# Optimization experiments

Hardware: AMD Instinct MI355X
Metric: run time of the kernel (lower is better)

## Reference

```python
import jax, jax.numpy as jnp
import numpy as np

N = 32768
NIN = 12
NC = 16
HID = 512
K = 8
B = 3.0
L = 8
D_HALF = NIN // 2                      # 6
DIN = D_HALF + NC                      # conditioner input
DOUT = (3 * K - 1) * (NIN - D_HALF)    # conditioner output
MIN_W = 1e-3
MIN_H = 1e-3
MIN_D = 1e-3
DERIV_CONST = float(np.log(np.exp(1.0 - MIN_D) - 1.0))  # softplus^{-1}(1-min_d)


def setup_inputs() -> dict:
    key = jax.random.key(0)
    ks = jax.random.split(key, 12)
    z = jax.random.normal(ks[0], (N, NIN), dtype=jnp.float32)
    c = jax.random.normal(ks[1], (N, NC), dtype=jnp.float32)

    def lin(k, fan_in, shape):
        bound = 1.0 / np.sqrt(fan_in)
        return jax.random.uniform(k, shape, jnp.float32, -bound, bound)

    W0 = lin(ks[2], DIN, (L, DIN, HID)); b0 = lin(ks[3], DIN, (L, HID))
    W1 = lin(ks[4], HID, (L, HID, HID)); b1 = lin(ks[5], HID, (L, HID))
    W2 = lin(ks[6], HID, (L, HID, HID)); b2 = lin(ks[7], HID, (L, HID))
    W3 = lin(ks[8], HID, (L, HID, DOUT)); b3 = lin(ks[9], HID, (L, DOUT))

    rng = np.random.default_rng(0)
    perms = jnp.asarray(np.stack([rng.permutation(NIN) for _ in range(L - 1)]),
                        dtype=jnp.int32)  # [L-1, NIN]
    return dict(z=z, c=c, W0=W0, b0=b0, W1=W1, b1=b1, W2=W2, b2=b2,
                W3=W3, b3=b3, perms=perms)


def _rqs(x, uw, uh, ud):
    """Unconstrained rational-quadratic spline (forward).
    x: [N, d2]; uw/uh: [N, d2, K]; ud: [N, d2, K+1] (already edge-padded)."""
    widths = jax.nn.softmax(uw, axis=-1)
    widths = MIN_W + (1.0 - MIN_W * K) * widths
    cw = jnp.cumsum(widths, axis=-1)
    cw = jnp.concatenate([jnp.zeros_like(cw[..., :1]), cw], axis=-1)
    cw = 2.0 * B * cw - B
    cw = cw.at[..., 0].set(-B).at[..., -1].set(B)
    w = cw[..., 1:] - cw[..., :-1]

    heights = jax.nn.softmax(uh, axis=-1)
    heights = MIN_H + (1.0 - MIN_H * K) * heights
    ch = jnp.cumsum(heights, axis=-1)
    ch = jnp.concatenate([jnp.zeros_like(ch[..., :1]), ch], axis=-1)
    ch = 2.0 * B * ch - B
    ch = ch.at[..., 0].set(-B).at[..., -1].set(B)
    h = ch[..., 1:] - ch[..., :-1]

    d = MIN_D + jax.nn.softplus(ud)  # [N, d2, K+1]

    xc = jnp.clip(x, -B, B)  # tails are handled by mask below
    # searchsorted: eps added only to the last knot for the search itself
    cw_search = cw.at[..., -1].add(1e-6)
    idx = jnp.clip(jnp.sum((xc[..., None] >= cw_search).astype(jnp.int32),
                           axis=-1) - 1, 0, K - 1)  # [N, d2]

    def g(a):
        return jnp.take_along_axis(a, idx[..., None], axis=-1)[..., 0]

    icw, iw = g(cw), g(w)
    ich, ih = g(ch), g(h)
    idelta = g(h / w)
    id0 = g(d)
    id1 = g(d[..., 1:])

    theta = (xc - icw) / iw
    t1m = theta * (1.0 - theta)
    num = ih * (idelta * theta**2 + id0 * t1m)
    den = idelta + (id0 + id1 - 2.0 * idelta) * t1m
    out = ich + num / den
    dnum = idelta**2 * (id1 * theta**2 + 2.0 * idelta * t1m
                        + id0 * (1.0 - theta)**2)
    lad = jnp.log(dnum) - 2.0 * jnp.log(den)

    inside = (x >= -B) & (x <= B)
    return jnp.where(inside, out, x), jnp.where(inside, lad, 0.0)


def _flow(z, c, W0, b0, W1, b1, W2, b2, W3, b3, perms):
    x = z
    total_ld = jnp.zeros(z.shape[0], dtype=z.dtype)
    for i in range(L):
        x1, x2 = x[:, :D_HALF], x[:, D_HALF:]
        inp = jnp.concatenate([x1, c], axis=-1)
        h0 = jax.nn.elu(inp @ W0[i] + b0[i])
        h1 = jax.nn.elu(h0 @ W1[i] + b1[i])
        h2 = jax.nn.elu(h1 @ W2[i] + b2[i])
        out = (h2 @ W3[i] + b3[i]).reshape(-1, NIN - D_HALF, 3 * K - 1)
        uw, uh, ud = out[..., :K], out[..., K:2 * K], out[..., 2 * K:]
        ud = jnp.pad(ud, ((0, 0), (0, 0), (1, 1)),
                     constant_values=DERIV_CONST)
        x2n, ld = _rqs(x2, uw, uh, ud)
        total_ld = total_ld + jnp.sum(ld, axis=-1)
        x = jnp.concatenate([x1, x2n], axis=-1)
        if i < L - 1:
            x = x[:, perms[i]]
    return x, total_ld


def reference(z, c, W0, b0, W1, b1, W2, b2, W3, b3, perms):
    return _flow(z, c, W0, b0, W1, b1, W2, b2, W3, b3, perms)
```

## Files before the change

kernel.cpp:

```cpp
#include <hip/hip_runtime.h>
#include <hip/hip_fp16.h>

#define NROWS   32768
#define MT      64
#define NTH     512
#define OS      148
#define BND     3.0f

typedef _Float16 half_t;
typedef __attribute__((ext_vector_type(8))) _Float16 f16x8;
typedef __attribute__((ext_vector_type(4))) _Float16 f16x4;
typedef __attribute__((ext_vector_type(4))) float    f32x4;


__global__ void pack_frag(const float* __restrict__ src, half_t* __restrict__ dst,
                          int K, int Nn, int NT, int KS) {
  int l = blockIdx.z;
  int frag = blockIdx.x * 4 + (threadIdx.x >> 6);
  int lane = threadIdx.x & 63;
  int NF = NT * KS;
  if (frag >= NF) return;
  int nt = frag / KS, ks = frag - nt * KS;
  int n = nt * 16 + (lane & 15);
  int kb = ks * 32 + (lane >> 4) * 8;
  f16x8 v;
#pragma unroll
  for (int e = 0; e < 8; e++) {
    int k = kb + e;
    v[e] = (k < K && n < Nn) ? (half_t)src[((size_t)l * K + k) * Nn + n] : (half_t)0.f;
  }
  *(f16x8*)(dst + ((size_t)l * NF + frag) * 512 + lane * 8) = v;
}

__device__ __forceinline__ float elu_f(float v) {
  return v > 0.f ? v : (__expf(v) - 1.f);
}

__device__ __forceinline__ void gemm_elu(
    const half_t* A, int KSA, int ksteps,
    const half_t* __restrict__ Wf, int KSW,
    const float* __restrict__ bias,
    half_t* dst,
    int w, int lane, int lm, int lk) {
  f16x8 a[2][4], b[2][4];
  f32x4 acc[4][4];
#pragma unroll
  for (int i = 0; i < 4; i++)
#pragma unroll
    for (int j = 0; j < 4; j++) acc[i][j] = (f32x4){0.f, 0.f, 0.f, 0.f};
  const int ntb = w * 4;

#pragma unroll
  for (int s = 0; s < 2; s++)
    if (s < ksteps) {
#pragma unroll
      for (int nt = 0; nt < 4; nt++)
        b[s][nt] = *(const f16x8*)(Wf + ((size_t)((ntb + nt) * KSW + s)) * 512 + lane * 8);
#pragma unroll
      for (int mf = 0; mf < 4; mf++)
        a[s][mf] = *(const f16x8*)(A + ((size_t)(mf * KSA + s)) * 512 + lane * 8);
    }

#pragma unroll
  for (int ks = 0; ks < ksteps; ks++) {
    const int sl = ks & 1;
#pragma unroll
    for (int nt = 0; nt < 4; nt++)
#pragma unroll
      for (int mf = 0; mf < 4; mf++)
        acc[mf][nt] = __builtin_amdgcn_mfma_f32_16x16x32_f16(b[sl][nt], a[sl][mf], acc[mf][nt], 0, 0, 0);
    if (ks + 2 < ksteps) {
#pragma unroll
      for (int nt = 0; nt < 4; nt++)
        b[sl][nt] = *(const f16x8*)(Wf + ((size_t)((ntb + nt) * KSW + ks + 2)) * 512 + lane * 8);
#pragma unroll
      for (int mf = 0; mf < 4; mf++)
        a[sl][mf] = *(const f16x8*)(A + ((size_t)(mf * KSA + ks + 2)) * 512 + lane * 8);
    }
  }
#pragma unroll
  for (int half = 0; half < 2; half++) {
    const int ksg = w * 2 + half;
#pragma unroll
    for (int ntl = 0; ntl < 2; ntl++) {
      int n0 = w * 64 + half * 32 + ntl * 16 + lk * 4;
      f32x4 bv = *(const f32x4*)(bias + n0);
      int lane_dst = (ntl * 2 + (lk >> 1)) * 16 + lm;
#pragma unroll
      for (int mf = 0; mf < 4; mf++) {
        f16x4 pv;
#pragma unroll
        for (int r = 0; r < 4; r++) pv[r] = (half_t)elu_f(acc[mf][half * 2 + ntl][r] + bv[r]);
        *(f16x4*)(dst + ((size_t)(mf * 16 + ksg)) * 512 + lane_dst * 8 + (lk & 1) * 4) = pv;
      }
    }
  }
}

__device__ __forceinline__ void gemm_out(
    const half_t* A,
    const half_t* __restrict__ Wf,
    const float* __restrict__ bias,
    float* outb,
    int w, int lane, int lm, int lk) {
  f32x4 acc[4][2];
#pragma unroll
  for (int i = 0; i < 4; i++)
#pragma unroll
    for (int j = 0; j < 2; j++) acc[i][j] = (f32x4){0.f, 0.f, 0.f, 0.f};
  const bool has2 = (w == 0);

  f16x8 a[2][4], b[4][2];
#pragma unroll
  for (int s = 0; s < 4; s++) {
    b[s][0] = *(const f16x8*)(Wf + ((size_t)(w * 16 + s)) * 512 + lane * 8);
    if (has2) b[s][1] = *(const f16x8*)(Wf + ((size_t)(8 * 16 + s)) * 512 + lane * 8);
  }
#pragma unroll
  for (int s = 0; s < 2; s++) {
#pragma unroll
    for (int mf = 0; mf < 4; mf++)
      a[s][mf] = *(const f16x8*)(A + ((size_t)(mf * 16 + s)) * 512 + lane * 8);
  }
#pragma unroll
  for (int ks = 0; ks < 16; ks++) {
    const int sl = ks & 3, asx = ks & 1;
#pragma unroll
    for (int mf = 0; mf < 4; mf++)
      acc[mf][0] = __builtin_amdgcn_mfma_f32_16x16x32_f16(b[sl][0], a[asx][mf], acc[mf][0], 0, 0, 0);
    if (has2)
#pragma unroll
      for (int mf = 0; mf < 4; mf++)
        acc[mf][1] = __builtin_amdgcn_mfma_f32_16x16x32_f16(b[sl][1], a[asx][mf], acc[mf][1], 0, 0, 0);
    if (ks + 4 < 16) {
      b[sl][0] = *(const f16x8*)(Wf + ((size_t)(w * 16 + ks + 4)) * 512 + lane * 8);
      if (has2) b[sl][1] = *(const f16x8*)(Wf + ((size_t)(128 + ks + 4)) * 512 + lane * 8);
    }
    if (ks + 2 < 16) {
#pragma unroll
      for (int mf = 0; mf < 4; mf++)
        a[asx][mf] = *(const f16x8*)(A + ((size_t)(mf * 16 + ks + 2)) * 512 + lane * 8);
    }
  }
  {
    int n0 = w * 16 + lk * 4;
    f32x4 bv = *(const f32x4*)(bias + n0);
#pragma unroll
    for (int mf = 0; mf < 4; mf++) {
      f32x4 ov = acc[mf][0] + bv;
      *(f32x4*)(outb + (mf * 16 + lm) * OS + n0) = ov;
    }
  }
  if (has2) {
    int n0 = 128 + lk * 4;
    f32x4 bv;
#pragma unroll
    for (int r = 0; r < 4; r++) bv[r] = (n0 + r < 138) ? bias[n0 + r] : 0.f;
#pragma unroll
    for (int mf = 0; mf < 4; mf++) {
      f32x4 ov = acc[mf][1] + bv;
      *(f32x4*)(outb + (mf * 16 + lm) * OS + n0) = ov;
    }
  }
}

__global__ __launch_bounds__(NTH, 2) __attribute__((amdgpu_waves_per_eu(2, 2)))
void flow_kernel(const float* __restrict__ z, const float* __restrict__ c,
                 const float* __restrict__ b0, const float* __restrict__ b1,
                 const float* __restrict__ b2, const float* __restrict__ b3,
                 const int* __restrict__ perms,
                 const half_t* __restrict__ W0F, const half_t* __restrict__ W1F,
                 const half_t* __restrict__ W2F, const half_t* __restrict__ W3F,
                 float* __restrict__ out) {
  __shared__ half_t hbufA[4 * 16 * 512];
  __shared__ __align__(16) char smemB[4 * 16 * 512 * 2];
  __shared__ half_t inpb[4 * 512];
  __shared__ half_t cbuf[MT * 16];
  __shared__ float xbuf[MT][12];
  __shared__ float ldpart[MT][6];
  __shared__ float ldtot[MT];
  __shared__ int   permbuf[7][12];

  half_t* hbufB  = (half_t*)smemB;
  float*  outbuf = (float*)smemB;

  int tid = threadIdx.x;
  int w = tid >> 6, lane = tid & 63;
  int lm = lane & 15, lk = lane >> 4;
  int row0 = blockIdx.x * MT;

  for (int it = tid; it < MT * 12; it += NTH) xbuf[it / 12][it % 12] = z[(size_t)row0 * 12 + it];
  for (int it = tid; it < MT * 16; it += NTH) cbuf[it] = (half_t)c[(size_t)row0 * 16 + it];
  for (int it = tid; it < 84; it += NTH) permbuf[it / 12][it % 12] = perms[it];
  if (tid < MT) ldtot[tid] = 0.f;
  __syncthreads();

  for (int l = 0; l < 8; l++) {
    for (int it = tid; it < MT * 32; it += NTH) {
      int m = it >> 5, k = it & 31;
      half_t bv;
      if (k < 6)       bv = (half_t)xbuf[m][k];
      else if (k < 22) bv = cbuf[m * 16 + (k - 6)];
      else             bv = (half_t)0.f;
      inpb[(m >> 4) * 512 + ((k >> 3) * 16 + (m & 15)) * 8 + (k & 7)] = bv;
    }
    __syncthreads();
    gemm_elu(inpb, 1, 1,   W0F + (size_t)l * 32 * 512,     1,  b0 + l * 512, hbufA, w, lane, lm, lk);
    __syncthreads();
    gemm_elu(hbufA, 16, 16, W1F + (size_t)l * 512 * 512,  16,  b1 + l * 512, hbufB, w, lane, lm, lk);
    __syncthreads();
    gemm_elu(hbufB, 16, 16, W2F + (size_t)l * 512 * 512,  16,  b2 + l * 512, hbufA, w, lane, lm, lk);
    __syncthreads();
    gemm_out(hbufA, W3F + (size_t)l * 144 * 512, b3 + l * 138, outbuf, w, lane, lm, lk);
    __syncthreads();

    if (tid < MT * 6) {
      int m = tid / 6, j = tid % 6;
      const float* pr = outbuf + m * OS + j * 23;
      float uw[8], uh[8], dd[9];
#pragma unroll
      for (int i = 0; i < 8; i++) uw[i] = pr[i];
#pragma unroll
      for (int i = 0; i < 8; i++) uh[i] = pr[8 + i];
      dd[0] = 1.f; dd[8] = 1.f;
#pragma unroll
      for (int i = 0; i < 7; i++) {
        float u = pr[16 + i];
        float sp = (u > 15.f) ? u : __logf(1.f + __expf(u));
        dd[i + 1] = 0.001f + sp;
      }
      float mw = uw[0];
#pragma unroll
      for (int i = 1; i < 8; i++) mw = fmaxf(mw, uw[i]);
      float ew[8], sw = 0.f;
#pragma unroll
      for (int i = 0; i < 8; i++) { ew[i] = __expf(uw[i] - mw); sw += ew[i]; }
      float invw = 1.f / sw;
      float cw[9]; cw[0] = -BND;
      float a = 0.f;
#pragma unroll
      for (int i = 0; i < 8; i++) { a += 0.001f + 0.992f * ew[i] * invw; cw[i + 1] = 2.f * BND * a - BND; }
      cw[8] = BND;
      float mh = uh[0];
#pragma unroll
      for (int i = 1; i < 8; i++) mh = fmaxf(mh, uh[i]);
      float eh[8], sh = 0.f;
#pragma unroll
      for (int i = 0; i < 8; i++) { eh[i] = __expf(uh[i] - mh); sh += eh[i]; }
      float invh = 1.f / sh;
      float ch[9]; ch[0] = -BND;
      float ah = 0.f;
#pragma unroll
      for (int i = 0; i < 8; i++) { ah += 0.001f + 0.992f * eh[i] * invh; ch[i + 1] = 2.f * BND * ah - BND; }
      ch[8] = BND;

      float x2 = xbuf[m][6 + j];
      float xc = fminf(fmaxf(x2, -BND), BND);
      int cnt = 0;
#pragma unroll
      for (int i = 0; i < 9; i++) {
        float edge = (i == 8) ? (cw[8] + 1e-6f) : cw[i];
        cnt += (xc >= edge) ? 1 : 0;
      }
      int idx = cnt - 1; idx = idx < 0 ? 0 : (idx > 7 ? 7 : idx);
      float icw = cw[0], iw = cw[1] - cw[0], ich = ch[0], ih = ch[1] - ch[0], d0 = dd[0], d1 = dd[1];
#pragma unroll
      for (int i = 0; i < 8; i++) {
        if (idx == i) {
          icw = cw[i]; iw = cw[i + 1] - cw[i];
          ich = ch[i]; ih = ch[i + 1] - ch[i];
          d0 = dd[i]; d1 = dd[i + 1];
        }
      }
      float delta = ih / iw;
      float th  = (xc - icw) / iw;
      float t1m = th * (1.f - th);
      float num = ih * (delta * th * th + d0 * t1m);
      float den = delta + (d0 + d1 - 2.f * delta) * t1m;
      float outv = ich + num / den;
      float dnum = delta * delta * (d1 * th * th + 2.f * delta * t1m + d0 * (1.f - th) * (1.f - th));
      float lad = __logf(dnum) - 2.f * __logf(den);
      bool inside = (x2 >= -BND) && (x2 <= BND);
      xbuf[m][6 + j] = inside ? outv : x2;
      ldpart[m][j]   = inside ? lad : 0.f;
    }
    __syncthreads();
    if (tid < MT) {
      float s = ldtot[tid];
#pragma unroll
      for (int j = 0; j < 6; j++) s += ldpart[tid][j];
      ldtot[tid] = s;
    }
    if (l < 7) {
      float v0 = xbuf[tid / 12][permbuf[l][tid % 12]];
      float v1 = 0.f;
      int it1 = tid + NTH;
      if (it1 < MT * 12) v1 = xbuf[it1 / 12][permbuf[l][it1 % 12]];
      __syncthreads();
      xbuf[tid / 12][tid % 12] = v0;
      if (it1 < MT * 12) xbuf[it1 / 12][it1 % 12] = v1;
    }
    __syncthreads();
  }

  for (int it = tid; it < MT * 12; it += NTH) out[(size_t)row0 * 12 + it] = xbuf[it / 12][it % 12];
  if (tid < MT) out[(size_t)NROWS * 12 + row0 + tid] = ldtot[tid];
}

extern "C" void kernel_launch(void* const* d_in, const int* in_sizes, int n_in,
                              void* d_out, int out_size, void* d_ws, size_t ws_size,
                              hipStream_t stream) {
  const float* z  = (const float*)d_in[0];
  const float* c  = (const float*)d_in[1];
  const float* W0 = (const float*)d_in[2];
  const float* b0 = (const float*)d_in[3];
  const float* W1 = (const float*)d_in[4];
  const float* b1 = (const float*)d_in[5];
  const float* W2 = (const float*)d_in[6];
  const float* b2 = (const float*)d_in[7];
  const float* W3 = (const float*)d_in[8];
  const float* b3 = (const float*)d_in[9];
  const int* perms = (const int*)d_in[10];

  unsigned short* wsu = (unsigned short*)d_ws;
  half_t* W0F = (half_t*)(wsu + 0);
  half_t* W1F = (half_t*)(wsu + 131072);
  half_t* W2F = (half_t*)(wsu + 2228224);
  half_t* W3F = (half_t*)(wsu + 4325376);

  pack_frag<<<dim3(8,   1, 8), dim3(256), 0, stream>>>(W0, W0F, 22,  512, 32, 1);
  pack_frag<<<dim3(128, 1, 8), dim3(256), 0, stream>>>(W1, W1F, 512, 512, 32, 16);
  pack_frag<<<dim3(128, 1, 8), dim3(256), 0, stream>>>(W2, W2F, 512, 512, 32, 16);
  pack_frag<<<dim3(36,  1, 8), dim3(256), 0, stream>>>(W3, W3F, 512, 138, 9,  16);

  flow_kernel<<<dim3(NROWS / MT), dim3(NTH), 0, stream>>>(
      z, c, b0, b1, b2, b3, perms, W0F, W1F, W2F, W3F, (float*)d_out);
}
```

Baseline: 501.0 us.

## Switch MLP GEMMs from 16x16x32 to 32x32x16 MFMA tiles

```diff
diff --git a/kernel.cpp b/kernel.cpp
--- a/kernel.cpp
+++ b/kernel.cpp
@@ -8,21 +8,22 @@
 #define BND     3.0f
 
 typedef _Float16 half_t;
-typedef __attribute__((ext_vector_type(8))) _Float16 f16x8;
-typedef __attribute__((ext_vector_type(4))) _Float16 f16x4;
-typedef __attribute__((ext_vector_type(4))) float    f32x4;
-
-
-__global__ void pack_frag(const float* __restrict__ src, half_t* __restrict__ dst,
-                          int K, int Nn, int NT, int KS) {
+typedef __attribute__((ext_vector_type(8)))  _Float16 f16x8;
+typedef __attribute__((ext_vector_type(4)))  _Float16 f16x4;
+typedef __attribute__((ext_vector_type(4)))  float    f32x4;
+typedef __attribute__((ext_vector_type(16))) float    f32x16;
+
+
+__global__ void pack_frag32(const float* __restrict__ src, half_t* __restrict__ dst,
+                            int K, int Nn, int NT, int KS) {
   int l = blockIdx.z;
   int frag = blockIdx.x * 4 + (threadIdx.x >> 6);
   int lane = threadIdx.x & 63;
   int NF = NT * KS;
   if (frag >= NF) return;
   int nt = frag / KS, ks = frag - nt * KS;
-  int n = nt * 16 + (lane & 15);
-  int kb = ks * 32 + (lane >> 4) * 8;
+  int n = nt * 32 + (lane & 31);
+  int kb = ks * 16 + (lane >> 5) * 8;
   f16x8 v;
 #pragma unroll
   for (int e = 0; e < 8; e++) {
@@ -37,61 +38,61 @@
 }
 
 __device__ __forceinline__ void gemm_elu(
-    const half_t* A, int KSA, int ksteps,
-    const half_t* __restrict__ Wf, int KSW,
+    const half_t* A, int ksteps,
+    const half_t* __restrict__ Wf,
     const float* __restrict__ bias,
     half_t* dst,
-    int w, int lane, int lm, int lk) {
-  f16x8 a[2][4], b[2][4];
-  f32x4 acc[4][4];
-#pragma unroll
-  for (int i = 0; i < 4; i++)
-#pragma unroll
-    for (int j = 0; j < 4; j++) acc[i][j] = (f32x4){0.f, 0.f, 0.f, 0.f};
-  const int ntb = w * 4;
-
-#pragma unroll
-  for (int s = 0; s < 2; s++)
-    if (s < ksteps) {
-#pragma unroll
-      for (int nt = 0; nt < 4; nt++)
-        b[s][nt] = *(const f16x8*)(Wf + ((size_t)((ntb + nt) * KSW + s)) * 512 + lane * 8);
-#pragma unroll
-      for (int mf = 0; mf < 4; mf++)
-        a[s][mf] = *(const f16x8*)(A + ((size_t)(mf * KSA + s)) * 512 + lane * 8);
-    }
+    int w, int lane) {
+  const int ml = lane & 31, hh = lane >> 5;
+  const int ntb = w * 2;
+  f16x8 a[2][2], b[2][2];
+  f32x16 acc[2][2];
+#pragma unroll
+  for (int i = 0; i < 2; i++)
+#pragma unroll
+    for (int j = 0; j < 2; j++)
+#pragma unroll
+      for (int r = 0; r < 16; r++) acc[i][j][r] = 0.f;
+
+#pragma unroll
+  for (int s = 0; s < 2; s++) {
+#pragma unroll
+    for (int ntl = 0; ntl < 2; ntl++)
+      b[s][ntl] = *(const f16x8*)(Wf + ((size_t)((ntb + ntl) * ksteps + s)) * 512 + lane * 8);
+#pragma unroll
+    for (int mf = 0; mf < 2; mf++)
+      a[s][mf] = *(const f16x8*)(A + ((size_t)(mf * ksteps + s)) * 512 + lane * 8);
+  }
 
 #pragma unroll
   for (int ks = 0; ks < ksteps; ks++) {
     const int sl = ks & 1;
-#pragma unroll
-    for (int nt = 0; nt < 4; nt++)
-#pragma unroll
-      for (int mf = 0; mf < 4; mf++)
-        acc[mf][nt] = __builtin_amdgcn_mfma_f32_16x16x32_f16(b[sl][nt], a[sl][mf], acc[mf][nt], 0, 0, 0);
+    acc[0][0] = __builtin_amdgcn_mfma_f32_32x32x16_f16(b[sl][0], a[sl][0], acc[0][0], 0, 0, 0);
+    acc[1][0] = __builtin_amdgcn_mfma_f32_32x32x16_f16(b[sl][0], a[sl][1], acc[1][0], 0, 0, 0);
+    acc[0][1] = __builtin_amdgcn_mfma_f32_32x32x16_f16(b[sl][1], a[sl][0], acc[0][1], 0, 0, 0);
+    acc[1][1] = __builtin_amdgcn_mfma_f32_32x32x16_f16(b[sl][1], a[sl][1], acc[1][1], 0, 0, 0);
     if (ks + 2 < ksteps) {
 #pragma unroll
-      for (int nt = 0; nt < 4; nt++)
-        b[sl][nt] = *(const f16x8*)(Wf + ((size_t)((ntb + nt) * KSW + ks + 2)) * 512 + lane * 8);
-#pragma unroll
-      for (int mf = 0; mf < 4; mf++)
-        a[sl][mf] = *(const f16x8*)(A + ((size_t)(mf * KSA + ks + 2)) * 512 + lane * 8);
-    }
-  }
-#pragma unroll
-  for (int half = 0; half < 2; half++) {
-    const int ksg = w * 2 + half;
+      for (int ntl = 0; ntl < 2; ntl++)
+        b[sl][ntl] = *(const f16x8*)(Wf + ((size_t)((ntb + ntl) * ksteps + ks + 2)) * 512 + lane * 8);
+#pragma unroll
+      for (int mf = 0; mf < 2; mf++)
+        a[sl][mf] = *(const f16x8*)(A + ((size_t)(mf * ksteps + ks + 2)) * 512 + lane * 8);
+    }
+  }
+#pragma unroll
+  for (int mf = 0; mf < 2; mf++) {
 #pragma unroll
     for (int ntl = 0; ntl < 2; ntl++) {
-      int n0 = w * 64 + half * 32 + ntl * 16 + lk * 4;
-      f32x4 bv = *(const f32x4*)(bias + n0);
-      int lane_dst = (ntl * 2 + (lk >> 1)) * 16 + lm;
-#pragma unroll
-      for (int mf = 0; mf < 4; mf++) {
+#pragma unroll
+      for (int g = 0; g < 4; g++) {
+        int kb = w * 64 + ntl * 32 + g * 8 + hh * 4;
+        f32x4 bv = *(const f32x4*)(bias + kb);
         f16x4 pv;
 #pragma unroll
-        for (int r = 0; r < 4; r++) pv[r] = (half_t)elu_f(acc[mf][half * 2 + ntl][r] + bv[r]);
-        *(f16x4*)(dst + ((size_t)(mf * 16 + ksg)) * 512 + lane_dst * 8 + (lk & 1) * 4) = pv;
+        for (int r = 0; r < 4; r++) pv[r] = (half_t)elu_f(acc[mf][ntl][g * 4 + r] + bv[r]);
+        *(f16x4*)(dst + ((size_t)(mf * 32 + (kb >> 4))) * 512
+                      + (ml + 32 * ((kb >> 3) & 1)) * 8 + (kb & 7)) = pv;
       }
     }
   }
@@ -102,64 +103,53 @@
     const half_t* __restrict__ Wf,
     const float* __restrict__ bias,
     float* outb,
-    int w, int lane, int lm, int lk) {
-  f32x4 acc[4][2];
-#pragma unroll
-  for (int i = 0; i < 4; i++)
-#pragma unroll
-    for (int j = 0; j < 2; j++) acc[i][j] = (f32x4){0.f, 0.f, 0.f, 0.f};
-  const bool has2 = (w == 0);
-
-  f16x8 a[2][4], b[4][2];
-#pragma unroll
-  for (int s = 0; s < 4; s++) {
-    b[s][0] = *(const f16x8*)(Wf + ((size_t)(w * 16 + s)) * 512 + lane * 8);
-    if (has2) b[s][1] = *(const f16x8*)(Wf + ((size_t)(8 * 16 + s)) * 512 + lane * 8);
-  }
+    int w, int lane) {
+  if (w >= 5) return;
+  const int ml = lane & 31, hh = lane >> 5;
+  f16x8 a[2][2], b[2];
+  f32x16 acc[2];
+#pragma unroll
+  for (int i = 0; i < 2; i++)
+#pragma unroll
+    for (int r = 0; r < 16; r++) acc[i][r] = 0.f;
+
 #pragma unroll
   for (int s = 0; s < 2; s++) {
-#pragma unroll
-    for (int mf = 0; mf < 4; mf++)
-      a[s][mf] = *(const f16x8*)(A + ((size_t)(mf * 16 + s)) * 512 + lane * 8);
-  }
-#pragma unroll
-  for (int ks = 0; ks < 16; ks++) {
-    const int sl = ks & 3, asx = ks & 1;
-#pragma unroll
-    for (int mf = 0; mf < 4; mf++)
-      acc[mf][0] = __builtin_amdgcn_mfma_f32_16x16x32_f16(b[sl][0], a[asx][mf], acc[mf][0], 0, 0, 0);
-    if (has2)
-#pragma unroll
-      for (int mf = 0; mf < 4; mf++)
-        acc[mf][1] = __builtin_amdgcn_mfma_f32_16x16x32_f16(b[sl][1], a[asx][mf], acc[mf][1], 0, 0, 0);
-    if (ks + 4 < 16) {
-      b[sl][0] = *(const f16x8*)(Wf + ((size_t)(w * 16 + ks + 4)) * 512 + lane * 8);
-      if (has2) b[sl][1] = *(const f16x8*)(Wf + ((size_t)(128 + ks + 4)) * 512 + lane * 8);
-    }
-    if (ks + 2 < 16) {
-#pragma unroll
-      for (int mf = 0; mf < 4; mf++)
-        a[asx][mf] = *(const f16x8*)(A + ((size_t)(mf * 16 + ks + 2)) * 512 + lane * 8);
-    }
-  }
-  {
-    int n0 = w * 16 + lk * 4;
-    f32x4 bv = *(const f32x4*)(bias + n0);
-#pragma unroll
-    for (int mf = 0; mf < 4; mf++) {
-      f32x4 ov = acc[mf][0] + bv;
-      *(f32x4*)(outb + (mf * 16 + lm) * OS + n0) = ov;
-    }
-  }
-  if (has2) {
-    int n0 = 128 + lk * 4;
-    f32x4 bv;
-#pragma unroll
-    for (int r = 0; r < 4; r++) bv[r] = (n0 + r < 138) ? bias[n0 + r] : 0.f;
-#pragma unroll
-    for (int mf = 0; mf < 4; mf++) {
-      f32x4 ov = acc[mf][1] + bv;
-      *(f32x4*)(outb + (mf * 16 + lm) * OS + n0) = ov;
+    b[s] = *(const f16x8*)(Wf + ((size_t)(w * 32 + s)) * 512 + lane * 8);
+#pragma unroll
+    for (int mf = 0; mf < 2; mf++)
+      a[s][mf] = *(const f16x8*)(A + ((size_t)(mf * 32 + s)) * 512 + lane * 8);
+  }
+#pragma unroll
+  for (int ks = 0; ks < 32; ks++) {
+    const int sl = ks & 1;
+    acc[0] = __builtin_amdgcn_mfma_f32_32x32x16_f16(b[sl], a[sl][0], acc[0], 0, 0, 0);
+    acc[1] = __builtin_amdgcn_mfma_f32_32x32x16_f16(b[sl], a[sl][1], acc[1], 0, 0, 0);
+    if (ks + 2 < 32) {
+      b[sl] = *(const f16x8*)(Wf + ((size_t)(w * 32 + ks + 2)) * 512 + lane * 8);
+#pragma unroll
+      for (int mf = 0; mf < 2; mf++)
+        a[sl][mf] = *(const f16x8*)(A + ((size_t)(mf * 32 + ks + 2)) * 512 + lane * 8);
+    }
+  }
+#pragma unroll
+  for (int mf = 0; mf < 2; mf++) {
+#pragma unroll
+    for (int g = 0; g < 4; g++) {
+      int nb = w * 32 + g * 8 + hh * 4;
+      if (nb < 145) {
+        f32x4 bv;
+        if (w < 4) {
+          bv = *(const f32x4*)(bias + nb);
+        } else {
+#pragma unroll
+          for (int r = 0; r < 4; r++) bv[r] = (nb + r < 138) ? bias[nb + r] : 0.f;
+        }
+        f32x4 ov;
+#pragma unroll
+        for (int r = 0; r < 4; r++) ov[r] = acc[mf][g * 4 + r] + bv[r];
+        *(f32x4*)(outb + (mf * 32 + ml) * OS + nb) = ov;
+      }
     }
   }
 }
@@ -172,9 +162,9 @@
                  const half_t* __restrict__ W0F, const half_t* __restrict__ W1F,
                  const half_t* __restrict__ W2F, const half_t* __restrict__ W3F,
                  float* __restrict__ out) {
-  __shared__ half_t hbufA[4 * 16 * 512];
-  __shared__ __align__(16) char smemB[4 * 16 * 512 * 2];
-  __shared__ half_t inpb[4 * 512];
+  __shared__ half_t hbufA[2 * 32 * 512];
+  __shared__ __align__(16) char smemB[2 * 32 * 512 * 2];
+  __shared__ half_t inpb[2 * 2 * 512];
   __shared__ half_t cbuf[MT * 16];
   __shared__ float xbuf[MT][12];
   __shared__ float ldpart[MT][6];
@@ -186,7 +176,6 @@
 
   int tid = threadIdx.x;
   int w = tid >> 6, lane = tid & 63;
-  int lm = lane & 15, lk = lane >> 4;
   int row0 = blockIdx.x * MT;
 
   for (int it = tid; it < MT * 12; it += NTH) xbuf[it / 12][it % 12] = z[(size_t)row0 * 12 + it];
@@ -202,16 +191,16 @@
       if (k < 6)       bv = (half_t)xbuf[m][k];
       else if (k < 22) bv = cbuf[m * 16 + (k - 6)];
       else             bv = (half_t)0.f;
-      inpb[(m >> 4) * 512 + ((k >> 3) * 16 + (m & 15)) * 8 + (k & 7)] = bv;
-    }
-    __syncthreads();
-    gemm_elu(inpb, 1, 1,   W0F + (size_t)l * 32 * 512,     1,  b0 + l * 512, hbufA, w, lane, lm, lk);
-    __syncthreads();
-    gemm_elu(hbufA, 16, 16, W1F + (size_t)l * 512 * 512,  16,  b1 + l * 512, hbufB, w, lane, lm, lk);
-    __syncthreads();
-    gemm_elu(hbufB, 16, 16, W2F + (size_t)l * 512 * 512,  16,  b2 + l * 512, hbufA, w, lane, lm, lk);
-    __syncthreads();
-    gemm_out(hbufA, W3F + (size_t)l * 144 * 512, b3 + l * 138, outbuf, w, lane, lm, lk);
+      inpb[((m >> 5) * 2 + (k >> 4)) * 512 + ((m & 31) + 32 * ((k >> 3) & 1)) * 8 + (k & 7)] = bv;
+    }
+    __syncthreads();
+    gemm_elu(inpb, 2,    W0F + (size_t)l * 32 * 512,   b0 + l * 512, hbufA, w, lane);
+    __syncthreads();
+    gemm_elu(hbufA, 32,  W1F + (size_t)l * 512 * 512,  b1 + l * 512, hbufB, w, lane);
+    __syncthreads();
+    gemm_elu(hbufB, 32,  W2F + (size_t)l * 512 * 512,  b2 + l * 512, hbufA, w, lane);
+    __syncthreads();
+    gemm_out(hbufA, W3F + (size_t)l * 160 * 512, b3 + l * 138, outbuf, w, lane);
     __syncthreads();
 
     if (tid < MT * 6) {
@@ -328,10 +317,10 @@
   half_t* W2F = (half_t*)(wsu + 2228224);
   half_t* W3F = (half_t*)(wsu + 4325376);
 
-  pack_frag<<<dim3(8,   1, 8), dim3(256), 0, stream>>>(W0, W0F, 22,  512, 32, 1);
-  pack_frag<<<dim3(128, 1, 8), dim3(256), 0, stream>>>(W1, W1F, 512, 512, 32, 16);
-  pack_frag<<<dim3(128, 1, 8), dim3(256), 0, stream>>>(W2, W2F, 512, 512, 32, 16);
-  pack_frag<<<dim3(36,  1, 8), dim3(256), 0, stream>>>(W3, W3F, 512, 138, 9,  16);
+  pack_frag32<<<dim3(8,   1, 8), dim3(256), 0, stream>>>(W0, W0F, 22,  512, 16, 2);
+  pack_frag32<<<dim3(128, 1, 8), dim3(256), 0, stream>>>(W1, W1F, 512, 512, 16, 32);
+  pack_frag32<<<dim3(128, 1, 8), dim3(256), 0, stream>>>(W2, W2F, 512, 512, 16, 32);
+  pack_frag32<<<dim3(40,  1, 8), dim3(256), 0, stream>>>(W3, W3F, 512, 138, 5,  32);
 
   flow_kernel<<<dim3(NROWS / MT), dim3(NTH), 0, stream>>>(
       z, c, b0, b1, b2, b3, perms, W0F, W1F, W2F, W3F, (float*)d_out);
```

Measured after the change: 548.9 us. 9.6% more time.
